# Optimization experiments

Measured on AMD Instinct MI355X. Metric: run time of the kernel, lower is better.

Reference implementation:

```python
import jax, jax.numpy as jnp
import numpy as np

B, N, D, H = 64, 196, 768, 3072
QMAX = 127.0  # 8-bit symmetric: clamp to [-128, 127]


def ste_round(x):
    # straight-through-estimator round (QAT)
    return x + jax.lax.stop_gradient(jnp.round(x) - x)


def q_linear_diag(x, w, b, a_sf):
    """Quantized diagonal linear (ResMLP Affine / LayerScale as QuantLinear)."""
    w_sf = jnp.max(jnp.abs(w)) / QMAX            # per-tensor weight scale
    w_int = ste_round(w / w_sf)                  # int8 weights (|.|<=127)
    out_int = (x / a_sf) * w_int
    if b is not None:
        out_int = out_int + ste_round(b / (a_sf * w_sf))  # 32-bit bias
    return out_int * (a_sf * w_sf), w_sf


def q_linear_dense(x, w, b, a_sf):
    """Quantized dense linear: int8 GEMM + int32 bias, dequant with a_sf*w_sf."""
    w_sf = jnp.max(jnp.abs(w)) / QMAX
    w_int = jnp.clip(ste_round(w / w_sf), -QMAX - 1, QMAX)
    out_int = jnp.einsum('...i,oi->...o', x / a_sf, w_int) + ste_round(b / (a_sf * w_sf))
    return out_int * (a_sf * w_sf), w_sf


def q_act(x, pre_sf, new_sf, identity=None, id_sf=None):
    """HAWQ-style QuantAct: fixed-point requantization to scale new_sf (8-bit)."""
    if identity is None:
        z_int = ste_round(x / pre_sf)
        out_int = ste_round(z_int * (pre_sf / new_sf))
    else:
        # main branch (x - identity) requantized with pre_sf, identity with id_sf
        z_int = ste_round((x - identity) / pre_sf)
        out_int = ste_round(z_int * (pre_sf / new_sf)) \
                + ste_round(ste_round(identity / id_sf) * (id_sf / new_sf))
    out_int = jnp.clip(out_int, -QMAX - 1, QMAX)
    return out_int * new_sf, new_sf


def _forward(x, norm1_w, norm1_b, attn_w, attn_b, gamma1_w,
             norm2_w, norm2_b, fc1_w, fc1_b, fc2_w, fc2_b, gamma2_w, act_sfs):
    a_sf = act_sfs[0]
    # --- token-mixing half ---
    identity, id_sf = x, a_sf
    x, w_sf = q_linear_diag(x, norm1_w, norm1_b, a_sf)         # norm1 (affine)
    x = jnp.swapaxes(x, 1, 2)                                  # [B, D, N]
    x, a_sf = q_act(x, a_sf * w_sf, act_sfs[1])                # quant_act1
    x, w_sf = q_linear_dense(x, attn_w, attn_b, a_sf)          # attn (cross-patch)
    x = jnp.swapaxes(x, 1, 2)                                  # [B, N, D]
    x, a_sf = q_act(x, a_sf * w_sf, act_sfs[2])                # quant_act2
    x, w_sf = q_linear_diag(x, gamma1_w, None, a_sf)           # gamma_1 (layerscale)
    x = x + identity
    x, a_sf = q_act(x, a_sf * w_sf, act_sfs[3], identity, id_sf)  # quant_act_int32_1
    # --- MLP half ---
    identity, id_sf = x, a_sf
    x, w_sf = q_linear_diag(x, norm2_w, norm2_b, a_sf)         # norm2
    x, a_sf = q_act(x, a_sf * w_sf, act_sfs[4])                # quant_act3
    x, w_sf = q_linear_dense(x, fc1_w, fc1_b, a_sf)            # mlp.fc1
    x = jax.nn.relu(x)
    x, a_sf = q_act(x, a_sf * w_sf, act_sfs[5])                # mlp.quant_act1
    x, w_sf = q_linear_dense(x, fc2_w, fc2_b, a_sf)            # mlp.fc2
    x, a_sf = q_act(x, a_sf * w_sf, act_sfs[6])                # mlp.quant_act2
    x, w_sf = q_linear_diag(x, gamma2_w, None, a_sf)           # gamma_2
    x = x + identity
    x, a_sf = q_act(x, a_sf * w_sf, act_sfs[7], identity, id_sf)  # quant_act_int32_2
    return x, a_sf


def setup_inputs() -> dict:
    key = jax.random.key(0)
    ks = jax.random.split(key, 16)
    act_sfs = jax.random.uniform(ks[14], (8,), jnp.float32, 0.02, 0.06)
    x = jax.random.normal(ks[0], (B, N, D), jnp.float32)
    # input is already quantized at scale act_sfs[0]
    x = jnp.clip(jnp.round(x / act_sfs[0]), -128, 127) * act_sfs[0]
    s = 0.05
    return {
        'x': x,
        'norm1_w': 1.0 + s * jax.random.normal(ks[1], (D,), jnp.float32),
        'norm1_b': s * jax.random.normal(ks[2], (D,), jnp.float32),
        'attn_w': jax.random.normal(ks[3], (N, N), jnp.float32) / np.sqrt(N),
        'attn_b': s * jax.random.normal(ks[4], (N,), jnp.float32),
        'gamma1_w': 0.1 + s * jax.random.normal(ks[5], (D,), jnp.float32),
        'norm2_w': 1.0 + s * jax.random.normal(ks[6], (D,), jnp.float32),
        'norm2_b': s * jax.random.normal(ks[7], (D,), jnp.float32),
        'fc1_w': jax.random.normal(ks[8], (H, D), jnp.float32) / np.sqrt(D),
        'fc1_b': s * jax.random.normal(ks[9], (H,), jnp.float32),
        'fc2_w': jax.random.normal(ks[10], (D, H), jnp.float32) / np.sqrt(H),
        'fc2_b': s * jax.random.normal(ks[11], (D,), jnp.float32),
        'gamma2_w': 0.1 + s * jax.random.normal(ks[12], (D,), jnp.float32),
        'act_sfs': act_sfs,
    }


def reference(x, norm1_w, norm1_b, attn_w, attn_b, gamma1_w,
              norm2_w, norm2_b, fc1_w, fc1_b, fc2_w, fc2_b, gamma2_w, act_sfs):
    return _forward(x, norm1_w, norm1_b, attn_w, attn_b, gamma1_w,
                    norm2_w, norm2_b, fc1_w, fc1_b, fc2_w, fc2_b, gamma2_w, act_sfs)
```

## Files before the change

### kernel.cpp

```cpp
#include <hip/hip_runtime.h>

#define B_ 64
#define N_ 196
#define D_ 768
#define H_ 3072
#define M_ (B_*N_)
#define NP 256

typedef int int4v  __attribute__((ext_vector_type(4)));
typedef int int16v __attribute__((ext_vector_type(16)));
typedef signed char i8;

#define WS_MAX 0
#define WS_W1F 16
#define WS_B1F (16+768)
#define WS_G1F (16+768*2)
#define WS_W2F (16+768*3)
#define WS_B2F (16+768*4)
#define WS_G2F (16+768*5)
#define WS_BA  (16+768*6)
#define WS_BF1 (WS_BA+256)
#define WS_BF2 (WS_BF1+3072)
#define OFF_WA   40960ull
#define OFF_FC1  (OFF_WA+65536ull)
#define OFF_FC2  (OFF_FC1+2359296ull)
#define OFF_X2   (OFF_FC2+2359296ull)
#define OFF_Q3   (OFF_X2+9633792ull)
#define OFF_Q4   (OFF_Q3+9633792ull)
#define OFF_Q1T  OFF_Q4
#define OFF_X8   (OFF_Q4+12582912ull)

__device__ __forceinline__ float clamp8(float v){ return fminf(fmaxf(v,-128.f),127.f); }

__device__ __forceinline__ void async16(const void* g, void* l){
    __builtin_amdgcn_global_load_lds((const __attribute__((address_space(1))) void*)g,
                                     (__attribute__((address_space(3))) void*)l, 16, 0, 0);
}

__global__ void k_init(char* ws, const float* __restrict__ act, float* out_tail){
    int id = blockIdx.x*256 + threadIdx.x;
    if (blockIdx.x == 0){
        float* f = (float*)ws;
        if (threadIdx.x < 8) f[WS_MAX+threadIdx.x] = 0.f;
        if (threadIdx.x == 8) *out_tail = act[7];
    }
    if (id < 4096){ int4v z = {0,0,0,0}; ((int4v*)(ws+OFF_WA))[id] = z; }
}

__global__ void k_maxabs(const float* __restrict__ p0, const float* __restrict__ p1,
                         const float* __restrict__ p2, const float* __restrict__ p3,
                         const float* __restrict__ p4, const float* __restrict__ p5,
                         const float* __restrict__ p6, float* wsmax){
    const float* ps[7] = {p0,p1,p2,p3,p4,p5,p6};
    const int    n4s[7] = {192, 9604, 192, 192, 589824, 589824, 192};
    int tid = blockIdx.y;
    const float4* p = (const float4*)ps[tid]; int n4 = n4s[tid];
    float m = 0.f;
    for (int i = blockIdx.x*blockDim.x + threadIdx.x; i < n4; i += gridDim.x*blockDim.x){
        float4 v = p[i];
        m = fmaxf(m, fmaxf(fmaxf(fabsf(v.x),fabsf(v.y)), fmaxf(fabsf(v.z),fabsf(v.w))));
    }
    #pragma unroll
    for (int off = 32; off; off >>= 1) m = fmaxf(m, __shfl_down(m, off, 64));
    __shared__ float red[4];
    int lane = threadIdx.x & 63, wv = threadIdx.x >> 6;
    if (lane == 0) red[wv] = m;
    __syncthreads();
    if (threadIdx.x == 0){
        float mm = red[0];
        for (int w = 1; w < (int)blockDim.x/64; w++) mm = fmaxf(mm, red[w]);
        atomicMax((unsigned*)&wsmax[tid], __float_as_uint(mm));
    }
}

__device__ __forceinline__ size_t cm_off(int o, int k, int KC){
    return (((size_t)(o>>7)*KC + (k>>6))<<13) + (((k>>4)&3)<<11) + ((o&127)<<4) + (k&15);
}

__global__ void k_qweights(const float* __restrict__ n1w, const float* __restrict__ n1b,
                           const float* __restrict__ aw,  const float* __restrict__ ab,
                           const float* __restrict__ g1w, const float* __restrict__ n2w,
                           const float* __restrict__ n2b, const float* __restrict__ f1w,
                           const float* __restrict__ f1b, const float* __restrict__ f2w,
                           const float* __restrict__ f2b, const float* __restrict__ g2w,
                           const float* __restrict__ act, char* ws){
    float* fws = (float*)ws;
    int*   iws = (int*)ws;
    const float* mx = fws + WS_MAX;
    long i = (long)blockIdx.x*blockDim.x + threadIdx.x;
    const long F4 = 589824;
    if (i < F4){ float sf = mx[4]/127.0f;
        float4 v = ((const float4*)f1w)[i];
        int o = (int)(i/192), kb = (int)(i%192)*4;
        unsigned b0 = (unsigned)(unsigned char)(i8)(int)fminf(fmaxf(rintf(v.x/sf),-128.f),127.f);
        unsigned b1 = (unsigned)(unsigned char)(i8)(int)fminf(fmaxf(rintf(v.y/sf),-128.f),127.f);
        unsigned b2 = (unsigned)(unsigned char)(i8)(int)fminf(fmaxf(rintf(v.z/sf),-128.f),127.f);
        unsigned b3 = (unsigned)(unsigned char)(i8)(int)fminf(fmaxf(rintf(v.w/sf),-128.f),127.f);
        *(unsigned*)(ws + OFF_FC1 + cm_off(o, kb, 12)) = b0 | (b1<<8) | (b2<<16) | (b3<<24);
        return; }
    i -= F4;
    if (i < F4){ float sf = mx[5]/127.0f;
        float4 v = ((const float4*)f2w)[i];
        int o = (int)(i/768), kb = (int)(i%768)*4;
        unsigned b0 = (unsigned)(unsigned char)(i8)(int)fminf(fmaxf(rintf(v.x/sf),-128.f),127.f);
        unsigned b1 = (unsigned)(unsigned char)(i8)(int)fminf(fmaxf(rintf(v.y/sf),-128.f),127.f);
        unsigned b2 = (unsigned)(unsigned char)(i8)(int)fminf(fmaxf(rintf(v.z/sf),-128.f),127.f);
        unsigned b3 = (unsigned)(unsigned char)(i8)(int)fminf(fmaxf(rintf(v.w/sf),-128.f),127.f);
        *(unsigned*)(ws + OFF_FC2 + cm_off(o, kb, 48)) = b0 | (b1<<8) | (b2<<16) | (b3<<24);
        return; }
    i -= F4;
    if (i < 38416){ float sf = mx[1]/127.0f;
        int o = (int)(i/196), k = (int)(i%196);
        ((i8*)(ws+OFF_WA))[cm_off(o, k, 4)] =
            (i8)(int)fminf(fmaxf(rintf(aw[i]/sf),-128.f),127.f); return; }
    i -= 38416;
    if (i < 768){ float sf = mx[0]/127.0f; fws[WS_W1F+i] = rintf(n1w[i]/sf); return; }
    i -= 768;
    if (i < 768){ float sf = mx[0]/127.0f; fws[WS_B1F+i] = rintf(n1b[i]/(act[0]*sf)); return; }
    i -= 768;
    if (i < 768){ float sf = mx[2]/127.0f; fws[WS_G1F+i] = rintf(g1w[i]/sf); return; }
    i -= 768;
    if (i < 768){ float sf = mx[3]/127.0f; fws[WS_W2F+i] = rintf(n2w[i]/sf); return; }
    i -= 768;
    if (i < 768){ float sf = mx[3]/127.0f; fws[WS_B2F+i] = rintf(n2b[i]/(act[3]*sf)); return; }
    i -= 768;
    if (i < 768){ float sf = mx[6]/127.0f; fws[WS_G2F+i] = rintf(g2w[i]/sf); return; }
    i -= 768;
    if (i < 196){ float sf = mx[1]/127.0f; iws[WS_BA+i] = (int)rintf(ab[i]/(act[1]*sf)); return; }
    i -= 196;
    if (i < 3072){ float sf = mx[4]/127.0f; iws[WS_BF1+i] = (int)rintf(f1b[i]/(act[4]*sf)); return; }
    i -= 3072;
    if (i < 768){ float sf = mx[5]/127.0f; iws[WS_BF2+i] = (int)rintf(f2b[i]/(act[5]*sf)); return; }
}

__global__ __launch_bounds__(256) void k_stage1(const float* __restrict__ x,
                                                const char* __restrict__ wsc,
                                                char* __restrict__ ws,
                                                const float* __restrict__ act){
    __shared__ i8 T[64][68];
    const float* fws = (const float*)wsc;
    int b = blockIdx.z, n0 = blockIdx.y*64, d0 = blockIdx.x*64;
    int t = threadIdx.x;
    float a0 = act[0];
    float w1sf = fws[WS_MAX+0]/127.0f;
    float r1 = (a0*w1sf)/act[1];
    int dl = (t & 15) * 4;
    int d  = d0 + dl;
    float4 wv = *(const float4*)(fws + WS_W1F + d);
    float4 bv = *(const float4*)(fws + WS_B1F + d);
    i8* x8 = (i8*)(ws + OFF_X8);
    #pragma unroll
    for (int pass = 0; pass < 4; pass++){
        int nl = (t >> 4) + pass*16;
        int n  = n0 + nl;
        i8 q[4] = {0,0,0,0};
        if (n < 196){
            float4 xv = *(const float4*)(x + ((size_t)b*196 + n)*768 + d);
            float i0 = rintf(xv.x/a0), i1 = rintf(xv.y/a0);
            float i2 = rintf(xv.z/a0), i3 = rintf(xv.w/a0);
            *(char4*)(x8 + ((size_t)b*196 + n)*768 + d) =
                make_char4((i8)(int)i0,(i8)(int)i1,(i8)(int)i2,(i8)(int)i3);
            float o0 = rintf(i0*wv.x + bv.x);
            float o1 = rintf(i1*wv.y + bv.y);
            float o2 = rintf(i2*wv.z + bv.z);
            float o3 = rintf(i3*wv.w + bv.w);
            q[0] = (i8)(int)clamp8(rintf(o0*r1));
            q[1] = (i8)(int)clamp8(rintf(o1*r1));
            q[2] = (i8)(int)clamp8(rintf(o2*r1));
            q[3] = (i8)(int)clamp8(rintf(o3*r1));
        }
        T[dl+0][nl] = q[0]; T[dl+1][nl] = q[1];
        T[dl+2][nl] = q[2]; T[dl+3][nl] = q[3];
    }
    __syncthreads();
    i8* q1T = (i8*)(ws + OFF_Q1T) + (size_t)b*196608;
    #pragma unroll
    for (int e = 0; e < 4; e++){
        int id = t + e*256;
        int row = id >> 4, c = (id & 15) * 4;
        int dd = d0 + row;
        int v = *(const int*)&T[row][c];
        size_t dst = (((size_t)(dd>>7)*4 + blockIdx.y)<<13) + ((size_t)(c>>4)<<11)
                     + ((dd&127)<<4) + (c&15);
        *(int*)(q1T + dst) = v;
    }
}

__device__ __forceinline__ void gemm_cm_256(const i8* __restrict__ gA, const i8* __restrict__ gB,
                                            int iters, int4v acc[4][4], i8* As, i8* Bs, int t){
    int lane = t & 63;
    int wm = (t>>6)&1, wn = t>>7;
    int lo = t*16;
    async16(gA + lo,        As + lo);
    async16(gA + 4096 + lo, As + 4096 + lo);
    async16(gB + lo,        Bs + lo);
    async16(gB + 4096 + lo, Bs + 4096 + lo);
    int arow = (lane>>4)*2048 + (wm*64 + (lane&15))*16;
    int brow = (lane>>4)*2048 + (wn*64 + (lane&15))*16;
    for (int i = 0; i < iters; i++){
        __syncthreads();
        if (i+1 < iters){
            int nb = ((i+1)&1) << 13;
            size_t kb = (size_t)(i+1) << 13;
            async16(gA + kb + lo,        As + nb + lo);
            async16(gA + kb + 4096 + lo, As + nb + 4096 + lo);
            async16(gB + kb + lo,        Bs + nb + lo);
            async16(gB + kb + 4096 + lo, Bs + nb + 4096 + lo);
        }
        int cb = (i&1) << 13;
        int4v a[4], bb[4];
        #pragma unroll
        for (int mt = 0; mt < 4; mt++)
            a[mt] = *(const int4v*)(As + cb + arow + mt*256);
        #pragma unroll
        for (int nt = 0; nt < 4; nt++)
            bb[nt] = *(const int4v*)(Bs + cb + brow + nt*256);
        #pragma unroll
        for (int mt = 0; mt < 4; mt++)
            #pragma unroll
            for (int nt = 0; nt < 4; nt++)
                acc[mt][nt] = __builtin_amdgcn_mfma_i32_16x16x64_i8(a[mt], bb[nt], acc[mt][nt], 0,0,0);
    }
}

__device__ __forceinline__ void gemm32_cm_256(const i8* __restrict__ gA, const i8* __restrict__ gB,
                                              int iters, int16v acc[2][2], i8* As, i8* Bs, int t){
    int lane = t & 63;
    int wm = (t>>6)&1, wn = t>>7;
    int lo = t*16;
    async16(gA + lo,        As + lo);
    async16(gA + 4096 + lo, As + 4096 + lo);
    async16(gB + lo,        Bs + lo);
    async16(gB + 4096 + lo, Bs + 4096 + lo);
    int arow = (lane>>5)*2048 + (wm*64 + (lane&31))*16;
    int brow = (lane>>5)*2048 + (wn*64 + (lane&31))*16;
    for (int i = 0; i < iters; i++){
        __syncthreads();
        if (i+1 < iters){
            int nb = ((i+1)&1) << 13;
            size_t kb = (size_t)(i+1) << 13;
            async16(gA + kb + lo,        As + nb + lo);
            async16(gA + kb + 4096 + lo, As + nb + 4096 + lo);
            async16(gB + kb + lo,        Bs + nb + lo);
            async16(gB + kb + 4096 + lo, Bs + nb + 4096 + lo);
        }
        int cb = (i&1) << 13;
        int4v a[2][2], bb[2][2];
        #pragma unroll
        for (int kk = 0; kk < 2; kk++){
            #pragma unroll
            for (int mt = 0; mt < 2; mt++){
                a[kk][mt]  = *(const int4v*)(As + cb + kk*4096 + arow + mt*512);
                bb[kk][mt] = *(const int4v*)(Bs + cb + kk*4096 + brow + mt*512);
            }
        }
        #pragma unroll
        for (int mt = 0; mt < 2; mt++)
            #pragma unroll
            for (int nt = 0; nt < 2; nt++)
                #pragma unroll
                for (int kk = 0; kk < 2; kk++)
                    acc[mt][nt] = __builtin_amdgcn_mfma_i32_32x32x32_i8(a[kk][mt], bb[kk][nt], acc[mt][nt], 0,0,0);
    }
}

__global__ __launch_bounds__(256) void k_attn(const char* __restrict__ ws,
                                              const float* __restrict__ act){
    __shared__ char smem[32768];
    const float* fws = (const float*)ws;
    const int*   iws = (const int*)ws;
    int b = blockIdx.z;
    int m0 = blockIdx.x*128, n0 = blockIdx.y*128;
    const i8* gA = (const i8*)(ws + OFF_WA)  + ((size_t)(m0>>7))*32768;
    const i8* gB = (const i8*)(ws + OFF_Q1T) + (size_t)b*196608 + ((size_t)(n0>>7))*32768;
    const i8* x8 = (const i8*)(ws + OFF_X8);
    i8* x2  = (i8*)(ws + OFF_X2);
    i8* q3  = (i8*)(ws + OFF_Q3);
    int t = threadIdx.x, lane = t & 63;
    int wm = (t>>6)&1, wn = t>>7;
    int4v acc[4][4]; int4v zz = {0,0,0,0};
    #pragma unroll
    for (int mt=0;mt<4;mt++) for (int nt=0;nt<4;nt++) acc[mt][nt] = zz;
    gemm_cm_256(gA, gB, 4, acc, (i8*)smem, (i8*)smem+16384, t);

    float a1=act[1], a2=act[2], a3=act[3], a4=act[4];
    float wasf = fws[WS_MAX+1]/127.0f; float r2  = (a1*wasf)/a2;
    float g1sf = fws[WS_MAX+2]/127.0f; float r3a = (a2*g1sf)/a3; float r3b = act[0]/a3;
    float w2sf = fws[WS_MAX+3]/127.0f; float r4  = (a3*w2sf)/a4;
    float g1v[4], w2v[4], b2v[4];
    #pragma unroll
    for (int nt=0;nt<4;nt++){
        int d = n0 + wn*64 + nt*16 + (lane&15);
        g1v[nt] = fws[WS_G1F + d]; w2v[nt] = fws[WS_W2F + d]; b2v[nt] = fws[WS_B2F + d];
    }
    __syncthreads();
    i8* Xs = (i8*)smem;
    i8* Qs = (i8*)smem + 16384;
    #pragma unroll
    for (int mt=0;mt<4;mt++){
        #pragma unroll
        for (int r=0;r<4;r++){
            int ml = wm*64 + mt*16 + (lane>>4)*4 + r;
            int o  = m0 + ml;
            int ba = iws[WS_BA + o];
            #pragma unroll
            for (int nt=0;nt<4;nt++){
                int nl = wn*64 + nt*16 + (lane&15);
                int d  = n0 + nl;
                float s2 = (float)(acc[mt][nt][r] + ba);
                float q2 = clamp8(rintf(s2*r2));
                float o3v = q2*g1v[nt];
                float idi = (o < 196) ? (float)x8[((size_t)b*196 + o)*768 + d] : 0.f;
                float tt = rintf(o3v*r3a) + rintf(idi*r3b);
                tt = clamp8(tt);
                float o4 = tt*w2v[nt] + b2v[nt];
                float qr = clamp8(rintf(o4*r4));
                Xs[ml*128 + nl] = (i8)(int)tt;
                Qs[ml*128 + nl] = (i8)(int)qr;
            }
        }
    }
    __syncthreads();
    #pragma unroll
    for (int e=0;e<4;e++){
        int id = t + e*256;
        int row = id>>3, c = id&7;
        int o = m0 + row;
        if (o < 196){
            int rg = b*196 + o;
            size_t g = (size_t)rg*768 + n0 + c*16;
            *(int4v*)(x2 + g) = *(const int4v*)(Xs + row*128 + c*16);
            size_t dst = (((size_t)(rg>>7)*12 + (n0>>6) + (c>>2))<<13)
                         + ((size_t)(c&3)<<11) + ((rg&127)<<4);
            *(int4v*)(q3 + dst) = *(const int4v*)(Qs + row*128 + c*16);
        }
    }
}

__global__ __launch_bounds__(256,4) void k_fc1(const char* __restrict__ ws, const float* __restrict__ act){
    __shared__ char smem[32768];
    const float* fws = (const float*)ws;
    const int*   iws = (const int*)ws;
    int n0 = blockIdx.y*128;
    const i8* gA = (const i8*)(ws+OFF_Q3)  + ((size_t)blockIdx.x)*12*8192;
    const i8* gB = (const i8*)(ws+OFF_FC1) + ((size_t)blockIdx.y)*12*8192;
    const int* bias = iws + WS_BF1;
    i8* q4 = (i8*)(ws+OFF_Q4);
    int t = threadIdx.x, lane = t & 63;
    int wm = (t>>6)&1, wn = t>>7;
    int16v acc[2][2];
    int16v zz = {0,0,0,0,0,0,0,0,0,0,0,0,0,0,0,0};
    #pragma unroll
    for (int mt=0;mt<2;mt++) for (int nt=0;nt<2;nt++) acc[mt][nt] = zz;
    gemm32_cm_256(gA, gB, 12, acc, (i8*)smem, (i8*)smem+16384, t);
    float wsf = fws[WS_MAX+4]/127.0f;
    float r5 = (act[4]*wsf)/act[5];
    int bcol[2];
    #pragma unroll
    for (int nt=0;nt<2;nt++) bcol[nt] = bias[n0 + wn*64 + nt*32 + (lane&31)];
    __syncthreads();
    i8* Cs = (i8*)smem;
    #pragma unroll
    for (int mt=0;mt<2;mt++){
        #pragma unroll
        for (int nt=0;nt<2;nt++){
            int nl = wn*64 + nt*32 + (lane&31);
            #pragma unroll
            for (int r=0;r<16;r++){
                int s = acc[mt][nt][r] + bcol[nt];
                if (s < 0) s = 0;
                float q = clamp8(rintf((float)s * r5));
                int ml = wm*64 + mt*32 + 4*(lane>>5) + (r&3) + 8*(r>>2);
                Cs[ml*128 + nl] = (i8)(int)q;
            }
        }
    }
    __syncthreads();
    #pragma unroll
    for (int e=0;e<4;e++){
        int id = t + e*256;
        int row = id>>3, c = id&7;
        size_t dst = (((size_t)blockIdx.x*48 + (n0>>6) + (c>>2))<<13)
                     + ((size_t)(c&3)<<11) + ((size_t)row<<4);
        *(int4v*)(q4 + dst) = *(const int4v*)(Cs + row*128 + c*16);
    }
}

__global__ __launch_bounds__(256,4) void k_fc2(const char* __restrict__ ws, const float* __restrict__ act,
                                               float* __restrict__ out){
    __shared__ char smem[32768];
    const float* fws = (const float*)ws;
    const int*   iws = (const int*)ws;
    int m0 = blockIdx.x*128, n0 = blockIdx.y*128;
    const i8* gA = (const i8*)(ws+OFF_Q4)  + ((size_t)blockIdx.x)*48*8192;
    const i8* gB = (const i8*)(ws+OFF_FC2) + ((size_t)blockIdx.y)*48*8192;
    const int* bias = iws + WS_BF2;
    const float* g2f = fws + WS_G2F;
    const i8* x2 = (const i8*)(ws+OFF_X2);
    int t = threadIdx.x, lane = t & 63;
    int wm = (t>>6)&1, wn = t>>7;
    int16v acc[2][2];
    int16v zz = {0,0,0,0,0,0,0,0,0,0,0,0,0,0,0,0};
    #pragma unroll
    for (int mt=0;mt<2;mt++) for (int nt=0;nt<2;nt++) acc[mt][nt] = zz;
    gemm32_cm_256(gA, gB, 48, acc, (i8*)smem, (i8*)smem+16384, t);
    float a3=act[3], a5=act[5], a6=act[6], a7=act[7];
    float wsf  = fws[WS_MAX+5]/127.0f; float r6  = (a5*wsf)/a6;
    float g2sf = fws[WS_MAX+6]/127.0f; float r7a = (a6*g2sf)/a7; float r7b = a3/a7;
    int bcol[2]; float g2v[2];
    #pragma unroll
    for (int nt=0;nt<2;nt++){
        int nc = n0 + wn*64 + nt*32 + (lane&31);
        bcol[nt] = bias[nc]; g2v[nt] = g2f[nc];
    }
    #pragma unroll
    for (int mt=0;mt<2;mt++){
        #pragma unroll
        for (int nt=0;nt<2;nt++){
            int nc = n0 + wn*64 + nt*32 + (lane&31);
            #pragma unroll
            for (int r=0;r<16;r++){
                int ml = wm*64 + mt*32 + 4*(lane>>5) + (r&3) + 8*(r>>2);
                size_t gi = (size_t)(m0+ml)*768 + nc;
                int s = acc[mt][nt][r] + bcol[nt];
                float q6 = clamp8(rintf((float)s*r6));
                float o7 = q6*g2v[nt];
                float idi = (float)x2[gi];
                float tt = rintf(o7*r7a) + rintf(idi*r7b);
                tt = clamp8(tt);
                out[gi] = tt*a7;
            }
        }
    }
}

extern "C" void kernel_launch(void* const* d_in, const int* in_sizes, int n_in,
                              void* d_out, int out_size, void* d_ws, size_t ws_size,
                              hipStream_t stream){
    const float* x   = (const float*)d_in[0];
    const float* n1w = (const float*)d_in[1];
    const float* n1b = (const float*)d_in[2];
    const float* aw  = (const float*)d_in[3];
    const float* ab  = (const float*)d_in[4];
    const float* g1w = (const float*)d_in[5];
    const float* n2w = (const float*)d_in[6];
    const float* n2b = (const float*)d_in[7];
    const float* f1w = (const float*)d_in[8];
    const float* f1b = (const float*)d_in[9];
    const float* f2w = (const float*)d_in[10];
    const float* f2b = (const float*)d_in[11];
    const float* g2w = (const float*)d_in[12];
    const float* act = (const float*)d_in[13];
    char* ws = (char*)d_ws;
    float* out = (float*)d_out;

    k_init<<<16,256,0,stream>>>(ws, act, out + (size_t)B_*N_*D_);
    k_maxabs<<<dim3(120,7),256,0,stream>>>(n1w, aw, g1w, n2w, f1w, f2w, g2w, (float*)ws);
    long qwThreads = 2L*589824 + 38416 + 768L*6 + 196 + 3072 + 768;
    k_qweights<<<(int)((qwThreads+255)/256),256,0,stream>>>(n1w,n1b,aw,ab,g1w,n2w,n2b,
                                                            f1w,f1b,f2w,f2b,g2w,act,ws);
    k_stage1<<<dim3(12,4,64),256,0,stream>>>(x, ws, ws, act);
    k_attn<<<dim3(2,6,64),256,0,stream>>>(ws, act);
    k_fc1<<<dim3(98,24),256,0,stream>>>(ws, act);
    k_fc2<<<dim3(98,6),256,0,stream>>>(ws, act, out);
}
```

Baseline: 261.8 us.

## Load GEMM fragments directly from global into registers, bypassing LDS staging

Replaces the LDS double-buffered async-copy GEMM mainloop used by fc1 and fc2 with a version where each wave loads its MFMA fragments straight from global memory into registers. A two-stage software pipeline overlaps the next k-slice loads with the current MFMAs. This drops the shared-memory traffic and the per-iteration barriers, and shrinks or removes LDS use, with launch bounds lowered to 3 blocks per CU. In exchange, operands shared between waves (the A tile across wn, the B tile across wm) are now fetched from global/L2 twice, and more registers are needed.

```diff
diff --git a/kernel.cpp b/kernel.cpp
--- a/kernel.cpp
+++ b/kernel.cpp
@@ -223,44 +223,39 @@
     }
 }
 
-__device__ __forceinline__ void gemm32_cm_256(const i8* __restrict__ gA, const i8* __restrict__ gB,
-                                              int iters, int16v acc[2][2], i8* As, i8* Bs, int t){
+struct Frag { int4v v[2][2]; };
+
+__device__ __forceinline__ void load_frag(Frag& f, const i8* __restrict__ p){
+    #pragma unroll
+    for (int kk = 0; kk < 2; kk++)
+        #pragma unroll
+        for (int m = 0; m < 2; m++)
+            f.v[kk][m] = *(const int4v*)(p + kk*4096 + m*512);
+}
+__device__ __forceinline__ void mfma8(int16v acc[2][2], const Frag& a, const Frag& b){
+    #pragma unroll
+    for (int mt = 0; mt < 2; mt++)
+        #pragma unroll
+        for (int nt = 0; nt < 2; nt++)
+            #pragma unroll
+            for (int kk = 0; kk < 2; kk++)
+                acc[mt][nt] = __builtin_amdgcn_mfma_i32_32x32x32_i8(a.v[kk][mt], b.v[kk][nt], acc[mt][nt], 0,0,0);
+}
+
+__device__ __forceinline__ void gemm32_direct(const i8* __restrict__ gA, const i8* __restrict__ gB,
+                                              int iters, int16v acc[2][2], int t){
     int lane = t & 63;
     int wm = (t>>6)&1, wn = t>>7;
-    int lo = t*16;
-    async16(gA + lo,        As + lo);
-    async16(gA + 4096 + lo, As + 4096 + lo);
-    async16(gB + lo,        Bs + lo);
-    async16(gB + 4096 + lo, Bs + 4096 + lo);
-    int arow = (lane>>5)*2048 + (wm*64 + (lane&31))*16;
-    int brow = (lane>>5)*2048 + (wn*64 + (lane&31))*16;
-    for (int i = 0; i < iters; i++){
-        __syncthreads();
-        if (i+1 < iters){
-            int nb = ((i+1)&1) << 13;
-            size_t kb = (size_t)(i+1) << 13;
-            async16(gA + kb + lo,        As + nb + lo);
-            async16(gA + kb + 4096 + lo, As + nb + 4096 + lo);
-            async16(gB + kb + lo,        Bs + nb + lo);
-            async16(gB + kb + 4096 + lo, Bs + nb + 4096 + lo);
-        }
-        int cb = (i&1) << 13;
-        int4v a[2][2], bb[2][2];
-        #pragma unroll
-        for (int kk = 0; kk < 2; kk++){
-            #pragma unroll
-            for (int mt = 0; mt < 2; mt++){
-                a[kk][mt]  = *(const int4v*)(As + cb + kk*4096 + arow + mt*512);
-                bb[kk][mt] = *(const int4v*)(Bs + cb + kk*4096 + brow + mt*512);
-            }
-        }
-        #pragma unroll
-        for (int mt = 0; mt < 2; mt++)
-            #pragma unroll
-            for (int nt = 0; nt < 2; nt++)
-                #pragma unroll
-                for (int kk = 0; kk < 2; kk++)
-                    acc[mt][nt] = __builtin_amdgcn_mfma_i32_32x32x32_i8(a[kk][mt], bb[kk][nt], acc[mt][nt], 0,0,0);
+    const i8* pA = gA + (lane>>5)*2048 + (wm*64 + (lane&31))*16;
+    const i8* pB = gB + (lane>>5)*2048 + (wn*64 + (lane&31))*16;
+    Frag a0, b0, a1, b1;
+    load_frag(a0, pA); load_frag(b0, pB);
+    for (int i = 0; i < iters; i += 2){
+        load_frag(a1, pA + 8192); load_frag(b1, pB + 8192);
+        mfma8(acc, a0, b0);
+        pA += 16384; pB += 16384;
+        if (i + 2 < iters){ load_frag(a0, pA); load_frag(b0, pB); }
+        mfma8(acc, a1, b1);
     }
 }
 
@@ -337,8 +332,8 @@
     }
 }
 
-__global__ __launch_bounds__(256,4) void k_fc1(const char* __restrict__ ws, const float* __restrict__ act){
-    __shared__ char smem[32768];
+__global__ __launch_bounds__(256,3) void k_fc1(const char* __restrict__ ws, const float* __restrict__ act){
+    __shared__ char smem[16384];
     const float* fws = (const float*)ws;
     const int*   iws = (const int*)ws;
     int n0 = blockIdx.y*128;
@@ -352,13 +347,12 @@
     int16v zz = {0,0,0,0,0,0,0,0,0,0,0,0,0,0,0,0};
     #pragma unroll
     for (int mt=0;mt<2;mt++) for (int nt=0;nt<2;nt++) acc[mt][nt] = zz;
-    gemm32_cm_256(gA, gB, 12, acc, (i8*)smem, (i8*)smem+16384, t);
+    gemm32_direct(gA, gB, 12, acc, t);
     float wsf = fws[WS_MAX+4]/127.0f;
     float r5 = (act[4]*wsf)/act[5];
     int bcol[2];
     #pragma unroll
     for (int nt=0;nt<2;nt++) bcol[nt] = bias[n0 + wn*64 + nt*32 + (lane&31)];
-    __syncthreads();
     i8* Cs = (i8*)smem;
     #pragma unroll
     for (int mt=0;mt<2;mt++){
@@ -386,9 +380,8 @@
     }
 }
 
-__global__ __launch_bounds__(256,4) void k_fc2(const char* __restrict__ ws, const float* __restrict__ act,
+__global__ __launch_bounds__(256,3) void k_fc2(const char* __restrict__ ws, const float* __restrict__ act,
                                                float* __restrict__ out){
-    __shared__ char smem[32768];
     const float* fws = (const float*)ws;
     const int*   iws = (const int*)ws;
     int m0 = blockIdx.x*128, n0 = blockIdx.y*128;
@@ -403,7 +396,7 @@
     int16v zz = {0,0,0,0,0,0,0,0,0,0,0,0,0,0,0,0};
     #pragma unroll
     for (int mt=0;mt<2;mt++) for (int nt=0;nt<2;nt++) acc[mt][nt] = zz;
-    gemm32_cm_256(gA, gB, 48, acc, (i8*)smem, (i8*)smem+16384, t);
+    gemm32_direct(gA, gB, 48, acc, t);
     float a3=act[3], a5=act[5], a6=act[6], a7=act[7];
     float wsf  = fws[WS_MAX+5]/127.0f; float r6  = (a5*wsf)/a6;
     float g2sf = fws[WS_MAX+6]/127.0f; float r7a = (a6*g2sf)/a7; float r7b = a3/a7;
```

After: 295.7 us. 1.13x slower.

## Triple-buffer LDS pipeline with explicit vmcnt waits in fc1/fc2 int8 GEMMs

Applied to the files above, without the earlier changes.

Replaces the double-buffered GEMM mainloop with a three-stage ring of LDS buffers. Two k-tiles are prefetched ahead, and each step waits with s_waitcnt vmcnt(4) plus a raw s_barrier instead of __syncthreads. This lets global-to-LDS copies overlap more MFMA work and hides load latency, and it also drops the barrier before the fc1 epilogue. The cost is 48KB of LDS per block, which lowers launch bounds occupancy from 4 to 3 blocks per CU.

```diff
diff --git a/kernel.cpp b/kernel.cpp
--- a/kernel.cpp
+++ b/kernel.cpp
@@ -223,35 +223,41 @@
     }
 }
 
-__device__ __forceinline__ void gemm32_cm_256(const i8* __restrict__ gA, const i8* __restrict__ gB,
-                                              int iters, int16v acc[2][2], i8* As, i8* Bs, int t){
+__device__ __forceinline__ void gemm32_cm_pipe(const i8* __restrict__ gA, const i8* __restrict__ gB,
+                                               int iters, int16v acc[2][2], i8* lds, int t){
     int lane = t & 63;
     int wm = (t>>6)&1, wn = t>>7;
     int lo = t*16;
-    async16(gA + lo,        As + lo);
-    async16(gA + 4096 + lo, As + 4096 + lo);
-    async16(gB + lo,        Bs + lo);
-    async16(gB + 4096 + lo, Bs + 4096 + lo);
+    auto stage = [&](int s, int buf){
+        size_t kb = (size_t)s << 13;
+        i8* L = lds + buf*16384;
+        async16(gA + kb + lo,        L + lo);
+        async16(gA + kb + 4096 + lo, L + 4096 + lo);
+        async16(gB + kb + lo,        L + 8192 + lo);
+        async16(gB + kb + 4096 + lo, L + 12288 + lo);
+    };
+    stage(0, 0);
+    if (iters > 1) stage(1, 1);
     int arow = (lane>>5)*2048 + (wm*64 + (lane&31))*16;
-    int brow = (lane>>5)*2048 + (wn*64 + (lane&31))*16;
+    int brow = 8192 + (lane>>5)*2048 + (wn*64 + (lane&31))*16;
+    int buf = 0;
     for (int i = 0; i < iters; i++){
-        __syncthreads();
-        if (i+1 < iters){
-            int nb = ((i+1)&1) << 13;
-            size_t kb = (size_t)(i+1) << 13;
-            async16(gA + kb + lo,        As + nb + lo);
-            async16(gA + kb + 4096 + lo, As + nb + 4096 + lo);
-            async16(gB + kb + lo,        Bs + nb + lo);
-            async16(gB + kb + 4096 + lo, Bs + nb + 4096 + lo);
-        }
-        int cb = (i&1) << 13;
+        if (i+1 < iters) asm volatile("s_waitcnt vmcnt(4)" ::: "memory");
+        else             asm volatile("s_waitcnt vmcnt(0)" ::: "memory");
+        __builtin_amdgcn_s_barrier();
+        __builtin_amdgcn_sched_barrier(0);
+        if (i+2 < iters){
+            int b2 = buf + 2; if (b2 >= 3) b2 -= 3;
+            stage(i+2, b2);
+        }
+        const i8* L = lds + buf*16384;
         int4v a[2][2], bb[2][2];
         #pragma unroll
         for (int kk = 0; kk < 2; kk++){
             #pragma unroll
             for (int mt = 0; mt < 2; mt++){
-                a[kk][mt]  = *(const int4v*)(As + cb + kk*4096 + arow + mt*512);
-                bb[kk][mt] = *(const int4v*)(Bs + cb + kk*4096 + brow + mt*512);
+                a[kk][mt]  = *(const int4v*)(L + kk*4096 + arow + mt*512);
+                bb[kk][mt] = *(const int4v*)(L + kk*4096 + brow + mt*512);
             }
         }
         #pragma unroll
@@ -261,6 +267,7 @@
                 #pragma unroll
                 for (int kk = 0; kk < 2; kk++)
                     acc[mt][nt] = __builtin_amdgcn_mfma_i32_32x32x32_i8(a[kk][mt], bb[kk][nt], acc[mt][nt], 0,0,0);
+        buf++; if (buf == 3) buf = 0;
     }
 }
 
@@ -337,8 +344,8 @@
     }
 }
 
-__global__ __launch_bounds__(256,4) void k_fc1(const char* __restrict__ ws, const float* __restrict__ act){
-    __shared__ char smem[32768];
+__global__ __launch_bounds__(256,3) void k_fc1(const char* __restrict__ ws, const float* __restrict__ act){
+    __shared__ char smem[49152];
     const float* fws = (const float*)ws;
     const int*   iws = (const int*)ws;
     int n0 = blockIdx.y*128;
@@ -352,13 +359,12 @@
     int16v zz = {0,0,0,0,0,0,0,0,0,0,0,0,0,0,0,0};
     #pragma unroll
     for (int mt=0;mt<2;mt++) for (int nt=0;nt<2;nt++) acc[mt][nt] = zz;
-    gemm32_cm_256(gA, gB, 12, acc, (i8*)smem, (i8*)smem+16384, t);
+    gemm32_cm_pipe(gA, gB, 12, acc, (i8*)smem, t);
     float wsf = fws[WS_MAX+4]/127.0f;
     float r5 = (act[4]*wsf)/act[5];
     int bcol[2];
     #pragma unroll
     for (int nt=0;nt<2;nt++) bcol[nt] = bias[n0 + wn*64 + nt*32 + (lane&31)];
-    __syncthreads();
     i8* Cs = (i8*)smem;
     #pragma unroll
     for (int mt=0;mt<2;mt++){
@@ -386,9 +392,9 @@
     }
 }
 
-__global__ __launch_bounds__(256,4) void k_fc2(const char* __restrict__ ws, const float* __restrict__ act,
+__global__ __launch_bounds__(256,3) void k_fc2(const char* __restrict__ ws, const float* __restrict__ act,
                                                float* __restrict__ out){
-    __shared__ char smem[32768];
+    __shared__ char smem[49152];
     const float* fws = (const float*)ws;
     const int*   iws = (const int*)ws;
     int m0 = blockIdx.x*128, n0 = blockIdx.y*128;
@@ -403,7 +409,7 @@
     int16v zz = {0,0,0,0,0,0,0,0,0,0,0,0,0,0,0,0};
     #pragma unroll
     for (int mt=0;mt<2;mt++) for (int nt=0;nt<2;nt++) acc[mt][nt] = zz;
-    gemm32_cm_256(gA, gB, 48, acc, (i8*)smem, (i8*)smem+16384, t);
+    gemm32_cm_pipe(gA, gB, 48, acc, (i8*)smem, t);
     float a3=act[3], a5=act[5], a6=act[6], a7=act[7];
     float wsf  = fws[WS_MAX+5]/127.0f; float r6  = (a5*wsf)/a6;
     float g2sf = fws[WS_MAX+6]/127.0f; float r7a = (a6*g2sf)/a7; float r7b = a3/a7;
```

After: 259.1 us. About the same (-1.0%).
